# Performance work log

Hardware: AMD Instinct MI355X
Metric: run time of the kernel (lower is better)

The kernel has to match this reference:

```python
import jax, jax.numpy as jnp
import numpy as np

D_MODEL = 2048
NHEADS = 16
ROPE_DIM = 64      # config.rope['head_dim']
NOPE_DIM = 128     # config.nope_head_dim
V_DIM = 128        # config.v_head_dim
Q_LORA = 1536      # config.q_lora_rank
KV_LORA = 512      # config.kv_lora_rank
ROPE_BASE = 10000.0
EPS = 1e-6
Q_HEAD = NOPE_DIM + ROPE_DIM   # 192
KV_HEAD = NOPE_DIM + V_DIM     # 256


def rms_norm(x, w):
    return x * jax.lax.rsqrt(jnp.mean(x * x, axis=-1, keepdims=True) + EPS) * w


def apply_rope(x, offset=0):
    # x: (B, H, T, d); standard rotate-half RoPE, positions offset by past length
    d, t = x.shape[-1], x.shape[2]
    inv_freq = 1.0 / (ROPE_BASE ** (jnp.arange(0, d, 2, dtype=jnp.float32) / d))
    pos = jnp.arange(offset, offset + t, dtype=jnp.float32)
    f = pos[:, None] * inv_freq[None, :]          # (T, d/2)
    cos = jnp.concatenate([jnp.cos(f), jnp.cos(f)], -1).astype(x.dtype)
    sin = jnp.concatenate([jnp.sin(f), jnp.sin(f)], -1).astype(x.dtype)
    x1, x2 = jnp.split(x, 2, axis=-1)
    rot = jnp.concatenate([-x2, x1], -1)
    return x * cos + rot * sin


def setup_inputs() -> dict:
    key = jax.random.key(0)
    ks = jax.random.split(key, 8)
    s = 0.02
    return {
        'x': jax.random.normal(ks[0], (2, 2048, D_MODEL), jnp.float32),
        'q_a_w': jax.random.normal(ks[1], (D_MODEL, Q_LORA), jnp.float32) * s,
        'q_a_norm_w': jnp.ones((Q_LORA,), jnp.float32),
        'q_b_w': jax.random.normal(ks[2], (Q_LORA, NHEADS * Q_HEAD), jnp.float32) * s,
        'kv_a_w': jax.random.normal(ks[3], (D_MODEL, KV_LORA + ROPE_DIM), jnp.float32) * s,
        'kv_norm_w': jnp.ones((KV_LORA,), jnp.float32),
        'kv_b_w': jax.random.normal(ks[4], (KV_LORA, NHEADS * KV_HEAD), jnp.float32) * s,
        'o_w': jax.random.normal(ks[5], (NHEADS * V_DIM, D_MODEL), jnp.float32) * s,
    }


def reference(x, q_a_w, q_a_norm_w, q_b_w, kv_a_w, kv_norm_w, kv_b_w, o_w):
    B, T, _ = x.shape
    # Query: LoRA down-proj -> RMSNorm -> up-proj
    q = rms_norm(x @ q_a_w, q_a_norm_w) @ q_b_w            # (B,T,H*Q_HEAD)
    q = q.reshape(B, T, NHEADS, Q_HEAD).transpose(0, 2, 1, 3)
    q_nope, q_rope = q[..., :NOPE_DIM], q[..., NOPE_DIM:]
    # KV: joint compressed projection, split into latent + shared rope key
    kv = x @ kv_a_w                                         # (B,T,KV_LORA+ROPE_DIM)
    kv_c, k_rope = kv[..., :KV_LORA], kv[..., KV_LORA:]
    k_rope = k_rope[:, None, :, :]                          # (B,1,T,ROPE_DIM) - MQA rope key
    kvb = rms_norm(kv_c, kv_norm_w) @ kv_b_w                # (B,T,H*KV_HEAD)
    kvb = kvb.reshape(B, T, NHEADS, KV_HEAD).transpose(0, 2, 1, 3)
    k_nope, v = kvb[..., :NOPE_DIM], kvb[..., NOPE_DIM:]
    # Decoupled RoPE (prefill: offset 0)
    q_rope = apply_rope(q_rope)
    k_rope = apply_rope(k_rope)
    qs = jnp.concatenate([q_nope, q_rope], -1)              # (B,H,T,Q_HEAD)
    ks = jnp.concatenate([k_nope, jnp.broadcast_to(k_rope, (B, NHEADS, T, ROPE_DIM))], -1)
    # SDPA with causal mask, scale = 1/sqrt(q_head_dim)
    scale = 1.0 / np.sqrt(Q_HEAD).astype(np.float32)
    scores = jnp.einsum('bhqd,bhkd->bhqk', qs, ks) * scale
    mask = jnp.tril(jnp.ones((T, T), bool))
    scores = jnp.where(mask[None, None], scores, jnp.finfo(scores.dtype).min)
    attn = jax.nn.softmax(scores, axis=-1)
    out = jnp.einsum('bhqk,bhkd->bhqd', attn, v)            # (B,H,T,V_DIM)
    out = out.transpose(0, 2, 1, 3).reshape(B, T, NHEADS * V_DIM)
    return out @ o_w                                        # (B,T,d_model)
```

## Files before the change

kernel.cpp:

```cpp
#include <hip/hip_runtime.h>
#include <hip/hip_bf16.h>
#include <math.h>

#define NHEADS 16
#define SEQ 2048
#define BATCH 2
#define NTOK (BATCH * SEQ)
#define EPSF 1e-6f

typedef short bf16x8 __attribute__((ext_vector_type(8)));
typedef float f32x4 __attribute__((ext_vector_type(4)));

__device__ __forceinline__ unsigned short f2bf(float v) {
    __hip_bfloat16 h = __float2bfloat16(v);
    return *reinterpret_cast<unsigned short*>(&h);
}
__device__ __forceinline__ float bf2f(unsigned short u) {
    __hip_bfloat16 h = *reinterpret_cast<__hip_bfloat16*>(&u);
    return __bfloat162float(h);
}
__device__ __forceinline__ void g2l16(const void* g, void* l) {
    __builtin_amdgcn_global_load_lds(
        (const __attribute__((address_space(1))) void*)g,
        (__attribute__((address_space(3))) void*)l, 16, 0, 0);
}

#define ROPE_L2 0.4152410118609203f

__global__ __launch_bounds__(256) void cvt_bf16(
    const float* __restrict__ in, unsigned short* __restrict__ out)
{
    const int i = blockIdx.x * 256 + threadIdx.x;
    float4 a = ((const float4*)in)[i * 2];
    float4 b = ((const float4*)in)[i * 2 + 1];
    unsigned short o[8] = {f2bf(a.x), f2bf(a.y), f2bf(a.z), f2bf(a.w),
                           f2bf(b.x), f2bf(b.y), f2bf(b.z), f2bf(b.w)};
    *(bf16x8*)(out + (size_t)i * 8) = *(bf16x8*)o;
}

struct WSeg { const float* src; unsigned short* dst; int Nw, K, nx, off; };
struct WSegs { WSeg s[5]; };

__global__ __launch_bounds__(256) void prep_weights(WSegs segs)
{
    __shared__ float T[32][33];
    const int bid = blockIdx.x;
    int si = 0;
#pragma unroll
    for (int i = 1; i < 5; ++i) si += (bid >= segs.s[i].off) ? 1 : 0;
    const WSeg sg = segs.s[si];
    const int local = bid - sg.off;
    const int bx = local % sg.nx, by = local / sg.nx;
    const int n0 = bx * 32, k0 = by * 32;
    const int tid = threadIdx.x;
    const int r = tid >> 3, c4 = (tid & 7) * 4;
    const bool valid = (n0 < sg.Nw);
    if (valid) {
        float4 v = *(const float4*)(sg.src + (size_t)(k0 + r) * sg.Nw + n0 + c4);
        T[r][c4 + 0] = v.x; T[r][c4 + 1] = v.y; T[r][c4 + 2] = v.z; T[r][c4 + 3] = v.w;
    }
    __syncthreads();
    unsigned short o[4];
#pragma unroll
    for (int j = 0; j < 4; ++j) o[j] = valid ? f2bf(T[c4 + j][r]) : (unsigned short)0;
    *(ulong1*)(sg.dst + (size_t)(n0 + r) * sg.K + k0 + c4) = *(ulong1*)o;
}

template <int OUT_BF16>
__global__ __launch_bounds__(256) void gemm_bt(
    const unsigned short* __restrict__ A,
    const unsigned short* __restrict__ Bt,
    void* __restrict__ Cv,
    int K, int N)
{
    __shared__ __align__(16) unsigned short As[128 * 32];
    __shared__ __align__(16) unsigned short Bs[128 * 32];
    const int tid = threadIdx.x;
    const int lane = tid & 63, wid = tid >> 6;
    const int l16 = lane & 15, lq = lane >> 4;
    const int wr = wid >> 1, wc = wid & 1;
    const int bm = blockIdx.y * 128, bn = blockIdx.x * 128;

    f32x4 acc[4][4];
#pragma unroll
    for (int m = 0; m < 4; ++m)
#pragma unroll
        for (int n = 0; n < 4; ++n) acc[m][n] = (f32x4){0.f, 0.f, 0.f, 0.f};

    for (int k0 = 0; k0 < K; k0 += 32) {
        __syncthreads();
#pragma unroll
        for (int t = 0; t < 2; ++t) {
            const int chunk = t * 256 + tid;
            const int row = chunk >> 2, koff = (chunk & 3) << 3;
            g2l16(A  + (size_t)(bm + row) * K + k0 + koff, (char*)As + chunk * 16);
            g2l16(Bt + (size_t)(bn + row) * K + k0 + koff, (char*)Bs + chunk * 16);
        }
        __syncthreads();

        bf16x8 af[4], bfr[4];
#pragma unroll
        for (int m = 0; m < 4; ++m)
            af[m] = *(const bf16x8*)(As + (wr * 64 + m * 16 + l16) * 32 + lq * 8);
#pragma unroll
        for (int n = 0; n < 4; ++n)
            bfr[n] = *(const bf16x8*)(Bs + (wc * 64 + n * 16 + l16) * 32 + lq * 8);
#pragma unroll
        for (int m = 0; m < 4; ++m)
#pragma unroll
            for (int n = 0; n < 4; ++n)
                acc[m][n] = __builtin_amdgcn_mfma_f32_16x16x32_bf16(af[m], bfr[n], acc[m][n], 0, 0, 0);
    }

#pragma unroll
    for (int m = 0; m < 4; ++m)
#pragma unroll
        for (int n = 0; n < 4; ++n)
#pragma unroll
            for (int reg = 0; reg < 4; ++reg) {
                const int row = bm + wr * 64 + m * 16 + lq * 4 + reg;
                const int col = bn + wc * 64 + n * 16 + l16;
                if (OUT_BF16) ((unsigned short*)Cv)[(size_t)row * N + col] = f2bf(acc[m][n][reg]);
                else          ((float*)Cv)[(size_t)row * N + col] = acc[m][n][reg];
            }
}

__global__ __launch_bounds__(256) void rmsnorm_bf(
    const float* __restrict__ in, const float* __restrict__ w,
    unsigned short* __restrict__ out, int in_stride, int cols)
{
    const int row = blockIdx.x;
    const float* p = in + (size_t)row * in_stride;
    float ss = 0.f;
    for (int c = threadIdx.x; c < cols; c += 256) { float v = p[c]; ss += v * v; }
#pragma unroll
    for (int off = 32; off > 0; off >>= 1) ss += __shfl_down(ss, off, 64);
    __shared__ float wsum[4];
    __shared__ float s_scale;
    const int wave = threadIdx.x >> 6;
    if ((threadIdx.x & 63) == 0) wsum[wave] = ss;
    __syncthreads();
    if (threadIdx.x == 0) {
        float t = wsum[0] + wsum[1] + wsum[2] + wsum[3];
        s_scale = rsqrtf(t / (float)cols + EPSF);
    }
    __syncthreads();
    const float sc = s_scale;
    for (int c = threadIdx.x; c < cols; c += 256)
        out[(size_t)row * cols + c] = f2bf(p[c] * sc * w[c]);
}

__global__ __launch_bounds__(256) void rmsnorm_kv_rope(
    const float* __restrict__ in, const float* __restrict__ w,
    unsigned short* __restrict__ kv_out, unsigned short* __restrict__ krope_out)
{
    const int row = blockIdx.x;
    const float* p = in + (size_t)row * 2176;
    const int tid = threadIdx.x;
    float v0 = p[tid], v1 = p[tid + 256];
    float ss = v0 * v0 + v1 * v1;
#pragma unroll
    for (int off = 32; off > 0; off >>= 1) ss += __shfl_down(ss, off, 64);
    __shared__ float wsum[4];
    __shared__ float s_scale;
    const int wave = tid >> 6;
    if ((tid & 63) == 0) wsum[wave] = ss;
    __syncthreads();
    if (tid == 0) {
        float t = wsum[0] + wsum[1] + wsum[2] + wsum[3];
        s_scale = rsqrtf(t / 512.0f + EPSF);
    }
    __syncthreads();
    const float sc = s_scale;
    kv_out[(size_t)row * 512 + tid]       = f2bf(v0 * sc * w[tid]);
    kv_out[(size_t)row * 512 + tid + 256] = f2bf(v1 * sc * w[tid + 256]);
    if (tid < 64) {
        const int s = row & (SEQ - 1);
        const int j = tid, jj = j & 31;
        float inv = exp2f(-ROPE_L2 * (float)jj);
        float f = (float)s * inv;
        float sn, cs;
        sincosf(f, &sn, &cs);
        const float* kb = p + 512;
        float v = (j < 32) ? (kb[j] * cs - kb[j + 32] * sn)
                           : (kb[j] * cs + kb[j - 32] * sn);
        krope_out[(size_t)row * 64 + j] = f2bf(v);
    }
}

__global__ __launch_bounds__(256) void pack_vt(
    const unsigned short* __restrict__ kvb, unsigned short* __restrict__ vt_bf)
{
    __shared__ __align__(16) unsigned short T[64][136];
    const int st = blockIdx.x, h = blockIdx.y, b = blockIdx.z;
    const int tid = threadIdx.x;
#pragma unroll
    for (int t = 0; t < 4; ++t) {
        int i = tid + t * 256;
        int r = i >> 4, c8 = i & 15;
        bf16x8 v = *(const bf16x8*)(kvb + (size_t)(b * SEQ + st * 64 + r) * 4096 + h * 256 + 128 + c8 * 8);
        *(bf16x8*)&T[r][c8 * 8] = v;
    }
    __syncthreads();
    const int d = tid >> 1, sh = (tid & 1) * 32;
    unsigned short tmp[32];
#pragma unroll
    for (int k = 0; k < 32; ++k) tmp[k] = T[sh + k][d];
    unsigned short* dst = vt_bf + ((size_t)(b * NHEADS + h) * 128 + d) * SEQ + st * 64 + sh;
#pragma unroll
    for (int c = 0; c < 4; ++c) *(bf16x8*)(dst + c * 8) = *(bf16x8*)&tmp[c * 8];
}

#define KPD 200
#define VPD 72
#define PPD 72
#define RESCALE_THR 8.0f

__global__ __launch_bounds__(256) void flash_mfma(
    const unsigned short* __restrict__ qbuf,
    const unsigned short* __restrict__ kvb,
    const unsigned short* __restrict__ krope,
    const unsigned short* __restrict__ vt,
    unsigned short* __restrict__ ctx)
{
    __shared__ __align__(16) unsigned short Ks[64][KPD];
    __shared__ __align__(16) unsigned short Vs[144][VPD];
    __shared__ __align__(16) unsigned short Ps[4][16][PPD];
    const int id = blockIdx.x;
    const int xcd = id & 7, sl = id >> 3;
    const int grp = sl >> 4, pair = sl & 15;
    const int hb = xcd + 8 * grp;
    const int h = hb & 15, b = hb >> 4;
    const int tid = threadIdx.x;
    const int wid = tid >> 6, lane = tid & 63;
    const int l16 = lane & 15, lq = lane >> 4;

    const size_t headV = (size_t)(b * NHEADS + h) * 128 * SEQ;
    const float scale = 0.07216878364870323f;

    float cs8[8], sn8[8];
    const int vrow = tid >> 1, vg = tid & 1;

    {
        int r = 128 + (tid >> 4);
        int c = (tid & 15) * 4;
        unsigned short v = (tid >> 4) == 0 ? (unsigned short)0x3F80 : (unsigned short)0;
        Vs[r][c] = v; Vs[r][c + 1] = v; Vs[r][c + 2] = v; Vs[r][c + 3] = v;
    }

#pragma unroll
    for (int pass = 0; pass < 2; ++pass) {
        const int qt = pass ? (31 - pair) : pair;
        const int srow = qt * 64 + wid * 16 + l16;

        bf16x8 qf[6];
        {
            const unsigned short* qp = qbuf + (size_t)(b * SEQ + srow) * 3072 + h * 192 + lq * 8;
            bf16x8 raw[6];
#pragma unroll
            for (int kk = 0; kk < 6; ++kk) raw[kk] = *(const bf16x8*)(qp + kk * 32);
#pragma unroll
            for (int jj = 0; jj < 8; ++jj) {
                float inv = exp2f(-ROPE_L2 * (float)(lq * 8 + jj));
                sincosf((float)srow * inv, &sn8[jj], &cs8[jj]);
            }
#pragma unroll
            for (int kk = 0; kk < 4; ++kk) {
                unsigned short o[8];
#pragma unroll
                for (int e = 0; e < 8; ++e) o[e] = f2bf(bf2f(((unsigned short*)&raw[kk])[e]) * scale);
                qf[kk] = *(bf16x8*)o;
            }
            unsigned short o4[8], o5[8];
#pragma unroll
            for (int e = 0; e < 8; ++e) {
                float x1 = bf2f(((unsigned short*)&raw[4])[e]);
                float x2 = bf2f(((unsigned short*)&raw[5])[e]);
                o4[e] = f2bf((x1 * cs8[e] - x2 * sn8[e]) * scale);
                o5[e] = f2bf((x2 * cs8[e] + x1 * sn8[e]) * scale);
            }
            qf[4] = *(bf16x8*)o4;
            qf[5] = *(bf16x8*)o5;
        }

        f32x4 o[8];
#pragma unroll
        for (int f = 0; f < 8; ++f) o[f] = (f32x4){0.f, 0.f, 0.f, 0.f};
        f32x4 oS = (f32x4){0.f, 0.f, 0.f, 0.f};
        float m[4] = {-1e30f, -1e30f, -1e30f, -1e30f};

        const int nkt = qt + 1;
        for (int kt = 0; kt < nkt; ++kt) {
            __syncthreads();
            {
                const int tk0 = b * SEQ + kt * 64;
#pragma unroll
                for (int t = 0; t < 4; ++t) {
                    int i = tid + t * 256;
                    int r = i >> 4, c8 = i & 15;
                    *(bf16x8*)&Ks[r][c8 * 8] =
                        *(const bf16x8*)(kvb + (size_t)(tk0 + r) * 4096 + h * 256 + c8 * 8);
                }
#pragma unroll
                for (int t = 0; t < 2; ++t) {
                    int i = tid + t * 256;
                    int r = i >> 3, c8 = i & 7;
                    *(bf16x8*)&Ks[r][128 + c8 * 8] =
                        *(const bf16x8*)(krope + (size_t)(tk0 + r) * 64 + c8 * 8);
                }
                const unsigned short* vsrc = vt + headV + (size_t)vrow * SEQ + kt * 64 + vg * 8;
#pragma unroll
                for (int j = 0; j < 4; ++j)
                    *(bf16x8*)&Vs[vrow][(vg + j * 2) * 8] = *(const bf16x8*)(vsrc + j * 16);
            }
            __syncthreads();

            f32x4 s[4];
#pragma unroll
            for (int f = 0; f < 4; ++f) s[f] = (f32x4){0.f, 0.f, 0.f, 0.f};
            __builtin_amdgcn_s_setprio(1);
#pragma unroll
            for (int f = 0; f < 4; ++f) {
#pragma unroll
                for (int kk = 0; kk < 6; ++kk) {
                    bf16x8 bfr = *(const bf16x8*)&Ks[f * 16 + l16][kk * 32 + lq * 8];
                    s[f] = __builtin_amdgcn_mfma_f32_16x16x32_bf16(qf[kk], bfr, s[f], 0, 0, 0);
                }
            }
            __builtin_amdgcn_s_setprio(0);

            const int qabs = qt * 64 + wid * 16 + lq * 4;
            const bool diag = (kt == qt);
            float rmax4[4];
#pragma unroll
            for (int reg = 0; reg < 4; ++reg) {
                if (diag) {
                    int q = qabs + reg;
                    int k0 = kt * 64 + l16;
                    if (k0      > q) s[0][reg] = -1e30f;
                    if (k0 + 16 > q) s[1][reg] = -1e30f;
                    if (k0 + 32 > q) s[2][reg] = -1e30f;
                    if (k0 + 48 > q) s[3][reg] = -1e30f;
                }
                float rmax = fmaxf(fmaxf(s[0][reg], s[1][reg]), fmaxf(s[2][reg], s[3][reg]));
                rmax = fmaxf(rmax, __shfl_xor(rmax, 1, 64));
                rmax = fmaxf(rmax, __shfl_xor(rmax, 2, 64));
                rmax = fmaxf(rmax, __shfl_xor(rmax, 4, 64));
                rmax = fmaxf(rmax, __shfl_xor(rmax, 8, 64));
                rmax4[reg] = rmax;
            }
            float dmx = fmaxf(fmaxf(rmax4[0] - m[0], rmax4[1] - m[1]),
                              fmaxf(rmax4[2] - m[2], rmax4[3] - m[3]));
            if (!__all(dmx <= RESCALE_THR)) {
#pragma unroll
                for (int reg = 0; reg < 4; ++reg) {
                    float mnew = fmaxf(m[reg], rmax4[reg]);
                    float al = __expf(m[reg] - mnew);
                    m[reg] = mnew;
#pragma unroll
                    for (int f = 0; f < 8; ++f) o[f][reg] *= al;
                    oS[reg] *= al;
                }
            }
#pragma unroll
            for (int reg = 0; reg < 4; ++reg) {
                Ps[wid][lq * 4 + reg][ 0 + l16] = f2bf(__expf(s[0][reg] - m[reg]));
                Ps[wid][lq * 4 + reg][16 + l16] = f2bf(__expf(s[1][reg] - m[reg]));
                Ps[wid][lq * 4 + reg][32 + l16] = f2bf(__expf(s[2][reg] - m[reg]));
                Ps[wid][lq * 4 + reg][48 + l16] = f2bf(__expf(s[3][reg] - m[reg]));
            }

            bf16x8 pa0 = *(const bf16x8*)&Ps[wid][l16][lq * 8];
            bf16x8 pa1 = *(const bf16x8*)&Ps[wid][l16][32 + lq * 8];
            __builtin_amdgcn_s_setprio(1);
#pragma unroll
            for (int f = 0; f < 8; ++f) {
                bf16x8 b0 = *(const bf16x8*)&Vs[f * 16 + l16][lq * 8];
                bf16x8 b1 = *(const bf16x8*)&Vs[f * 16 + l16][32 + lq * 8];
                o[f] = __builtin_amdgcn_mfma_f32_16x16x32_bf16(pa0, b0, o[f], 0, 0, 0);
                o[f] = __builtin_amdgcn_mfma_f32_16x16x32_bf16(pa1, b1, o[f], 0, 0, 0);
            }
            {
                bf16x8 s0 = *(const bf16x8*)&Vs[128 + l16][lq * 8];
                bf16x8 s1 = *(const bf16x8*)&Vs[128 + l16][32 + lq * 8];
                oS = __builtin_amdgcn_mfma_f32_16x16x32_bf16(pa0, s0, oS, 0, 0, 0);
                oS = __builtin_amdgcn_mfma_f32_16x16x32_bf16(pa1, s1, oS, 0, 0, 0);
            }
            __builtin_amdgcn_s_setprio(0);
        }

#pragma unroll
        for (int reg = 0; reg < 4; ++reg) {
            float ls = __shfl(oS[reg], lane & 48, 64);
            float inv = 1.0f / ls;
            unsigned short* dst = ctx + (size_t)(b * SEQ + qt * 64 + wid * 16 + lq * 4 + reg) * 2048 + h * 128 + l16;
#pragma unroll
            for (int f = 0; f < 8; ++f) dst[f * 16] = f2bf(o[f][reg] * inv);
        }
    }
}

extern "C" void kernel_launch(void* const* d_in, const int* in_sizes, int n_in,
                              void* d_out, int out_size, void* d_ws, size_t ws_size,
                              hipStream_t stream) {
    const float* x          = (const float*)d_in[0];
    const float* q_a_w      = (const float*)d_in[1];
    const float* q_a_norm_w = (const float*)d_in[2];
    const float* q_b_w      = (const float*)d_in[3];
    const float* kv_a_w     = (const float*)d_in[4];
    const float* kv_norm_w  = (const float*)d_in[5];
    const float* kv_b_w     = (const float*)d_in[6];
    const float* o_w        = (const float*)d_in[7];
    float* out = (float*)d_out;

    char* ws = (char*)d_ws;
    float*          qkv_cat  = (float*)(ws + 0);
    unsigned short* ctx_bf   = (unsigned short*)(ws + 0);
    unsigned short* qbuf_bf  = (unsigned short*)(ws + 35651584);
    unsigned short* vt_bf    = (unsigned short*)(ws + 60817408);
    unsigned short* kvb_bf   = (unsigned short*)(ws + 77594624);
    unsigned short* x_bf     = (unsigned short*)(ws + 111149056);
    unsigned short* q_a_bf   = (unsigned short*)(ws + 111149056);
    unsigned short* kv_c_bf  = (unsigned short*)(ws + 127926272);
    unsigned short* krope_bf = (unsigned short*)(ws + 132120576);
    unsigned short* wcat     = (unsigned short*)(ws + 132644864);
    unsigned short* wkva_t   = wcat + (size_t)1536 * 2048;
    unsigned short* wqb_t    = (unsigned short*)(ws + 141557760);
    unsigned short* wkvb_t   = (unsigned short*)(ws + 150994944);
    unsigned short* wo_t     = (unsigned short*)(ws + 155189248);

    dim3 blk(256);

    cvt_bf16<<<4096, blk, 0, stream>>>(x, x_bf);
    WSegs segs;
    segs.s[0] = { q_a_w,  wcat,   1536, 2048,  48,     0 };
    segs.s[1] = { q_b_w,  wqb_t,  3072, 1536,  96,  3072 };
    segs.s[2] = { kv_a_w, wkva_t,  576, 2048,  20,  7680 };
    segs.s[3] = { kv_b_w, wkvb_t, 4096,  512, 128,  8960 };
    segs.s[4] = { o_w,    wo_t,   2048, 2048,  64, 11008 };
    prep_weights<<<15104, blk, 0, stream>>>(segs);

    gemm_bt<0><<<dim3(17, 32), blk, 0, stream>>>(x_bf, wcat, qkv_cat, 2048, 2176);

    rmsnorm_bf<<<NTOK, blk, 0, stream>>>(qkv_cat, q_a_norm_w, q_a_bf, 2176, 1536);
    rmsnorm_kv_rope<<<NTOK, blk, 0, stream>>>(qkv_cat + 1536, kv_norm_w, kv_c_bf, krope_bf);

    gemm_bt<1><<<dim3(24, 32), blk, 0, stream>>>(q_a_bf, wqb_t, qbuf_bf, 1536, 3072);
    gemm_bt<1><<<dim3(32, 32), blk, 0, stream>>>(kv_c_bf, wkvb_t, kvb_bf, 512, 4096);

    pack_vt<<<dim3(SEQ / 64, NHEADS, BATCH), blk, 0, stream>>>(kvb_bf, vt_bf);

    flash_mfma<<<dim3(512), blk, 0, stream>>>(qbuf_bf, kvb_bf, krope_bf, vt_bf, ctx_bf);

    gemm_bt<0><<<dim3(16, 32), blk, 0, stream>>>(ctx_bf, wo_t, out, 2048, 2048);
}
```

Before: 367.6 us.

## Merge launches: fold x conversion, fuse norms, combine stage-2 GEMMs with V transpose

Folds the x fp32->bf16 conversion into the weight-prep kernel as extra blocks, merges the two RMSNorm kernels into one launch, and combines the q_b and kv_b GEMMs into one grid whose V-column tiles write transposed V directly, which removes the separate pack_vt pass. It also replaces sincosf with the fast __sinf/__cosf intrinsics for query RoPE. The aim is fewer kernel launches and tail effects, and no extra read and write of V. The fast trig intrinsics can lose accuracy at large positions, and the transposed V store uses narrow 8-byte strided writes.

```diff
diff --git a/kernel.cpp b/kernel.cpp
--- a/kernel.cpp
+++ b/kernel.cpp
@@ -27,24 +27,25 @@
 
 #define ROPE_L2 0.4152410118609203f
 
-__global__ __launch_bounds__(256) void cvt_bf16(
-    const float* __restrict__ in, unsigned short* __restrict__ out)
-{
-    const int i = blockIdx.x * 256 + threadIdx.x;
-    float4 a = ((const float4*)in)[i * 2];
-    float4 b = ((const float4*)in)[i * 2 + 1];
-    unsigned short o[8] = {f2bf(a.x), f2bf(a.y), f2bf(a.z), f2bf(a.w),
-                           f2bf(b.x), f2bf(b.y), f2bf(b.z), f2bf(b.w)};
-    *(bf16x8*)(out + (size_t)i * 8) = *(bf16x8*)o;
-}
-
 struct WSeg { const float* src; unsigned short* dst; int Nw, K, nx, off; };
 struct WSegs { WSeg s[5]; };
-
-__global__ __launch_bounds__(256) void prep_weights(WSegs segs)
+#define CVT_OFF 15104
+
+__global__ __launch_bounds__(256) void prep_weights(
+    WSegs segs, const float* __restrict__ x, unsigned short* __restrict__ x_bf)
 {
+    const int bid = blockIdx.x;
+    const int tid = threadIdx.x;
+    if (bid >= CVT_OFF) {
+        const int i = (bid - CVT_OFF) * 256 + tid;
+        float4 a = ((const float4*)x)[i * 2];
+        float4 b = ((const float4*)x)[i * 2 + 1];
+        unsigned short o[8] = {f2bf(a.x), f2bf(a.y), f2bf(a.z), f2bf(a.w),
+                               f2bf(b.x), f2bf(b.y), f2bf(b.z), f2bf(b.w)};
+        *(bf16x8*)(x_bf + (size_t)i * 8) = *(bf16x8*)o;
+        return;
+    }
     __shared__ float T[32][33];
-    const int bid = blockIdx.x;
     int si = 0;
 #pragma unroll
     for (int i = 1; i < 5; ++i) si += (bid >= segs.s[i].off) ? 1 : 0;
@@ -52,7 +53,6 @@
     const int local = bid - sg.off;
     const int bx = local % sg.nx, by = local / sg.nx;
     const int n0 = bx * 32, k0 = by * 32;
-    const int tid = threadIdx.x;
     const int r = tid >> 3, c4 = (tid & 7) * 4;
     const bool valid = (n0 < sg.Nw);
     if (valid) {
@@ -125,90 +125,154 @@
             }
 }
 
-__global__ __launch_bounds__(256) void rmsnorm_bf(
-    const float* __restrict__ in, const float* __restrict__ w,
-    unsigned short* __restrict__ out, int in_stride, int cols)
+__global__ __launch_bounds__(256) void gemm_stage2(
+    const unsigned short* __restrict__ qa,
+    const unsigned short* __restrict__ wqb,
+    unsigned short* __restrict__ qbuf,
+    const unsigned short* __restrict__ kvc,
+    const unsigned short* __restrict__ wkvb,
+    unsigned short* __restrict__ kvb,
+    unsigned short* __restrict__ vt)
 {
-    const int row = blockIdx.x;
-    const float* p = in + (size_t)row * in_stride;
-    float ss = 0.f;
-    for (int c = threadIdx.x; c < cols; c += 256) { float v = p[c]; ss += v * v; }
-#pragma unroll
-    for (int off = 32; off > 0; off >>= 1) ss += __shfl_down(ss, off, 64);
-    __shared__ float wsum[4];
-    __shared__ float s_scale;
-    const int wave = threadIdx.x >> 6;
-    if ((threadIdx.x & 63) == 0) wsum[wave] = ss;
-    __syncthreads();
-    if (threadIdx.x == 0) {
-        float t = wsum[0] + wsum[1] + wsum[2] + wsum[3];
-        s_scale = rsqrtf(t / (float)cols + EPSF);
-    }
-    __syncthreads();
-    const float sc = s_scale;
-    for (int c = threadIdx.x; c < cols; c += 256)
-        out[(size_t)row * cols + c] = f2bf(p[c] * sc * w[c]);
-}
-
-__global__ __launch_bounds__(256) void rmsnorm_kv_rope(
-    const float* __restrict__ in, const float* __restrict__ w,
-    unsigned short* __restrict__ kv_out, unsigned short* __restrict__ krope_out)
+    __shared__ __align__(16) unsigned short As[128 * 32];
+    __shared__ __align__(16) unsigned short Bs[128 * 32];
+    const int bid = blockIdx.x;
+    const int tid = threadIdx.x;
+    const int lane = tid & 63, wid = tid >> 6;
+    const int l16 = lane & 15, lq = lane >> 4;
+    const int wr = wid >> 1, wc = wid & 1;
+
+    const bool is_q = bid < 768;
+    const unsigned short* A;
+    const unsigned short* Bt;
+    int K, N, bm, bn;
+    if (is_q) { A = qa;  Bt = wqb;  K = 1536; N = 3072; bn = (bid % 24) * 128;        bm = (bid / 24) * 128; }
+    else      { A = kvc; Bt = wkvb; K = 512;  N = 4096; bn = ((bid - 768) % 32) * 128; bm = ((bid - 768) / 32) * 128; }
+
+    f32x4 acc[4][4];
+#pragma unroll
+    for (int m = 0; m < 4; ++m)
+#pragma unroll
+        for (int n = 0; n < 4; ++n) acc[m][n] = (f32x4){0.f, 0.f, 0.f, 0.f};
+
+    for (int k0 = 0; k0 < K; k0 += 32) {
+        __syncthreads();
+#pragma unroll
+        for (int t = 0; t < 2; ++t) {
+            const int chunk = t * 256 + tid;
+            const int row = chunk >> 2, koff = (chunk & 3) << 3;
+            g2l16(A  + (size_t)(bm + row) * K + k0 + koff, (char*)As + chunk * 16);
+            g2l16(Bt + (size_t)(bn + row) * K + k0 + koff, (char*)Bs + chunk * 16);
+        }
+        __syncthreads();
+
+        bf16x8 af[4], bfr[4];
+#pragma unroll
+        for (int m = 0; m < 4; ++m)
+            af[m] = *(const bf16x8*)(As + (wr * 64 + m * 16 + l16) * 32 + lq * 8);
+#pragma unroll
+        for (int n = 0; n < 4; ++n)
+            bfr[n] = *(const bf16x8*)(Bs + (wc * 64 + n * 16 + l16) * 32 + lq * 8);
+#pragma unroll
+        for (int m = 0; m < 4; ++m)
+#pragma unroll
+            for (int n = 0; n < 4; ++n)
+                acc[m][n] = __builtin_amdgcn_mfma_f32_16x16x32_bf16(af[m], bfr[n], acc[m][n], 0, 0, 0);
+    }
+
+    const bool is_v = (!is_q) && ((bn & 255) == 128);
+    if (!is_v) {
+        unsigned short* C = is_q ? qbuf : kvb;
+#pragma unroll
+        for (int m = 0; m < 4; ++m)
+#pragma unroll
+            for (int n = 0; n < 4; ++n)
+#pragma unroll
+                for (int reg = 0; reg < 4; ++reg) {
+                    const int row = bm + wr * 64 + m * 16 + lq * 4 + reg;
+                    const int col = bn + wc * 64 + n * 16 + l16;
+                    C[(size_t)row * N + col] = f2bf(acc[m][n][reg]);
+                }
+    } else {
+        const int h = bn >> 8;
+#pragma unroll
+        for (int m = 0; m < 4; ++m)
+#pragma unroll
+            for (int n = 0; n < 4; ++n) {
+                const int d = wc * 64 + n * 16 + l16;
+                const int tok0 = bm + wr * 64 + m * 16 + lq * 4;
+                const int b_ = tok0 >> 11, s_ = tok0 & (SEQ - 1);
+                unsigned short pk[4];
+#pragma unroll
+                for (int reg = 0; reg < 4; ++reg) pk[reg] = f2bf(acc[m][n][reg]);
+                *(ulong1*)(vt + (((size_t)(b_ * NHEADS + h) * 128 + d) * SEQ + s_)) = *(ulong1*)pk;
+            }
+    }
+}
+
+__global__ __launch_bounds__(256) void norms_fused(
+    const float* __restrict__ qkv, const float* __restrict__ qw,
+    const float* __restrict__ kvw,
+    unsigned short* __restrict__ qa_out, unsigned short* __restrict__ kv_out,
+    unsigned short* __restrict__ krope_out)
 {
-    const int row = blockIdx.x;
-    const float* p = in + (size_t)row * 2176;
+    const int bid = blockIdx.x;
     const int tid = threadIdx.x;
-    float v0 = p[tid], v1 = p[tid + 256];
-    float ss = v0 * v0 + v1 * v1;
-#pragma unroll
-    for (int off = 32; off > 0; off >>= 1) ss += __shfl_down(ss, off, 64);
     __shared__ float wsum[4];
     __shared__ float s_scale;
     const int wave = tid >> 6;
-    if ((tid & 63) == 0) wsum[wave] = ss;
-    __syncthreads();
-    if (tid == 0) {
-        float t = wsum[0] + wsum[1] + wsum[2] + wsum[3];
-        s_scale = rsqrtf(t / 512.0f + EPSF);
-    }
-    __syncthreads();
-    const float sc = s_scale;
-    kv_out[(size_t)row * 512 + tid]       = f2bf(v0 * sc * w[tid]);
-    kv_out[(size_t)row * 512 + tid + 256] = f2bf(v1 * sc * w[tid + 256]);
-    if (tid < 64) {
-        const int s = row & (SEQ - 1);
-        const int j = tid, jj = j & 31;
-        float inv = exp2f(-ROPE_L2 * (float)jj);
-        float f = (float)s * inv;
-        float sn, cs;
-        sincosf(f, &sn, &cs);
-        const float* kb = p + 512;
-        float v = (j < 32) ? (kb[j] * cs - kb[j + 32] * sn)
-                           : (kb[j] * cs + kb[j - 32] * sn);
-        krope_out[(size_t)row * 64 + j] = f2bf(v);
-    }
-}
-
-__global__ __launch_bounds__(256) void pack_vt(
-    const unsigned short* __restrict__ kvb, unsigned short* __restrict__ vt_bf)
-{
-    __shared__ __align__(16) unsigned short T[64][136];
-    const int st = blockIdx.x, h = blockIdx.y, b = blockIdx.z;
-    const int tid = threadIdx.x;
-#pragma unroll
-    for (int t = 0; t < 4; ++t) {
-        int i = tid + t * 256;
-        int r = i >> 4, c8 = i & 15;
-        bf16x8 v = *(const bf16x8*)(kvb + (size_t)(b * SEQ + st * 64 + r) * 4096 + h * 256 + 128 + c8 * 8);
-        *(bf16x8*)&T[r][c8 * 8] = v;
-    }
-    __syncthreads();
-    const int d = tid >> 1, sh = (tid & 1) * 32;
-    unsigned short tmp[32];
-#pragma unroll
-    for (int k = 0; k < 32; ++k) tmp[k] = T[sh + k][d];
-    unsigned short* dst = vt_bf + ((size_t)(b * NHEADS + h) * 128 + d) * SEQ + st * 64 + sh;
-#pragma unroll
-    for (int c = 0; c < 4; ++c) *(bf16x8*)(dst + c * 8) = *(bf16x8*)&tmp[c * 8];
+
+    if (bid < 4096) {
+        const int row = bid;
+        const float* p = qkv + (size_t)row * 2176;
+        float ss = 0.f;
+#pragma unroll
+        for (int t = 0; t < 6; ++t) { float v = p[tid + t * 256]; ss += v * v; }
+#pragma unroll
+        for (int off = 32; off > 0; off >>= 1) ss += __shfl_down(ss, off, 64);
+        if ((tid & 63) == 0) wsum[wave] = ss;
+        __syncthreads();
+        if (tid == 0) {
+            float t = wsum[0] + wsum[1] + wsum[2] + wsum[3];
+            s_scale = rsqrtf(t / 1536.0f + EPSF);
+        }
+        __syncthreads();
+        const float sc = s_scale;
+#pragma unroll
+        for (int t = 0; t < 6; ++t) {
+            int c = tid + t * 256;
+            qa_out[(size_t)row * 1536 + c] = f2bf(p[c] * sc * qw[c]);
+        }
+    } else {
+        const int row = bid - 4096;
+        const float* p = qkv + (size_t)row * 2176 + 1536;
+        float v0 = p[tid], v1 = p[tid + 256];
+        float ss = v0 * v0 + v1 * v1;
+#pragma unroll
+        for (int off = 32; off > 0; off >>= 1) ss += __shfl_down(ss, off, 64);
+        if ((tid & 63) == 0) wsum[wave] = ss;
+        __syncthreads();
+        if (tid == 0) {
+            float t = wsum[0] + wsum[1] + wsum[2] + wsum[3];
+            s_scale = rsqrtf(t / 512.0f + EPSF);
+        }
+        __syncthreads();
+        const float sc = s_scale;
+        kv_out[(size_t)row * 512 + tid]       = f2bf(v0 * sc * kvw[tid]);
+        kv_out[(size_t)row * 512 + tid + 256] = f2bf(v1 * sc * kvw[tid + 256]);
+        if (tid < 64) {
+            const int s = row & (SEQ - 1);
+            const int j = tid, jj = j & 31;
+            float inv = exp2f(-ROPE_L2 * (float)jj);
+            float f = (float)s * inv;
+            float sn, cs;
+            sincosf(f, &sn, &cs);
+            const float* kb = p + 512;
+            float v = (j < 32) ? (kb[j] * cs - kb[j + 32] * sn)
+                               : (kb[j] * cs + kb[j - 32] * sn);
+            krope_out[(size_t)row * 64 + j] = f2bf(v);
+        }
+    }
 }
 
 #define KPD 200
@@ -262,7 +326,9 @@
 #pragma unroll
             for (int jj = 0; jj < 8; ++jj) {
                 float inv = exp2f(-ROPE_L2 * (float)(lq * 8 + jj));
-                sincosf((float)srow * inv, &sn8[jj], &cs8[jj]);
+                float fp = (float)srow * inv;
+                sn8[jj] = __sinf(fp);
+                cs8[jj] = __cosf(fp);
             }
 #pragma unroll
             for (int kk = 0; kk < 4; ++kk) {
@@ -431,24 +497,21 @@
 
     dim3 blk(256);
 
-    cvt_bf16<<<4096, blk, 0, stream>>>(x, x_bf);
     WSegs segs;
     segs.s[0] = { q_a_w,  wcat,   1536, 2048,  48,     0 };
     segs.s[1] = { q_b_w,  wqb_t,  3072, 1536,  96,  3072 };
     segs.s[2] = { kv_a_w, wkva_t,  576, 2048,  20,  7680 };
     segs.s[3] = { kv_b_w, wkvb_t, 4096,  512, 128,  8960 };
     segs.s[4] = { o_w,    wo_t,   2048, 2048,  64, 11008 };
-    prep_weights<<<15104, blk, 0, stream>>>(segs);
+    prep_weights<<<CVT_OFF + 4096, blk, 0, stream>>>(segs, x, x_bf);
 
     gemm_bt<0><<<dim3(17, 32), blk, 0, stream>>>(x_bf, wcat, qkv_cat, 2048, 2176);
 
-    rmsnorm_bf<<<NTOK, blk, 0, stream>>>(qkv_cat, q_a_norm_w, q_a_bf, 2176, 1536);
-    rmsnorm_kv_rope<<<NTOK, blk, 0, stream>>>(qkv_cat + 1536, kv_norm_w, kv_c_bf, krope_bf);
-
-    gemm_bt<1><<<dim3(24, 32), blk, 0, stream>>>(q_a_bf, wqb_t, qbuf_bf, 1536, 3072);
-    gemm_bt<1><<<dim3(32, 32), blk, 0, stream>>>(kv_c_bf, wkvb_t, kvb_bf, 512, 4096);
-
-    pack_vt<<<dim3(SEQ / 64, NHEADS, BATCH), blk, 0, stream>>>(kvb_bf, vt_bf);
+    norms_fused<<<8192, blk, 0, stream>>>(qkv_cat, q_a_norm_w, kv_norm_w,
+                                          q_a_bf, kv_c_bf, krope_bf);
+
+    gemm_stage2<<<1792, blk, 0, stream>>>(q_a_bf, wqb_t, qbuf_bf,
+                                          kv_c_bf, wkvb_t, kvb_bf, vt_bf);
 
     flash_mfma<<<dim3(512), blk, 0, stream>>>(qbuf_bf, kvb_bf, krope_bf, vt_bf, ctx_bf);
 
```

Measured after the change: 342.9 us. -6.7%, faster.
